# Kernel optimization log

Hardware: AMD Instinct MI355X
Metric: run time of the kernel (lower is better)

Reference implementation:

```python
import jax, jax.numpy as jnp
import numpy as np

IN_C, OUT_C = 128, 256
KH, KW = 3, 3
STRIDE = (1, 1)
PAD = (1, 1)


def setup_inputs() -> dict:
    key = jax.random.key(0)
    kx, kw = jax.random.split(key)
    x = jax.random.normal(kx, (32, IN_C, 56, 56), dtype=jnp.float32)
    k = 1.0 / (IN_C * KH * KW)
    weight = (2.0 * jax.random.uniform(kw, (OUT_C, IN_C, KH, KW), dtype=jnp.float32) - 1.0) * (k ** 0.5)
    return {"x": x, "weight": weight}


def reference(x, weight):
    # Equivalent to the as_strided broadcast-multiply-sum: a plain 2D cross-correlation
    # (no bias), NCHW input, OIHW weight, stride (1,1), padding (1,1).
    return jax.lax.conv_general_dilated(
        x, weight,
        window_strides=STRIDE,
        padding=[(PAD[0], PAD[0]), (PAD[1], PAD[1])],
        dimension_numbers=("NCHW", "OIHW", "NCHW"),
    )
```

## Files before the change

### kernel.cpp

```cpp
#include <hip/hip_runtime.h>

typedef __attribute__((ext_vector_type(8))) short short8;
typedef __attribute__((ext_vector_type(4))) float floatx4;

#define IN_C 128
#define OUT_C 256
#define NB 32
#define HW 56
#define S_PER_N (HW * HW)
#define M_TOTAL (NB * S_PER_N)
#define PH 58
#define PW 66
#define XN_ELEMS (NB * PH * PW * IN_C)
#define WT_ELEMS (9 * OUT_C * IN_C)
#define XF_BLOCKS (PH * NB)
#define WF_BLOCKS (WT_ELEMS / 256)

__device__ __forceinline__ unsigned short f2bf(float f) {
    unsigned int u = __builtin_bit_cast(unsigned int, f);
    u = (u + 0x7FFFu + ((u >> 16) & 1u)) >> 16;
    return (unsigned short)u;
}

__device__ __forceinline__ void gld_lds16(const unsigned short* g, unsigned short* l) {
    __builtin_amdgcn_global_load_lds(
        (const __attribute__((address_space(1))) unsigned int*)g,
        (__attribute__((address_space(3))) unsigned int*)l, 16, 0, 0);
}

__global__ void xform_all(const float* __restrict__ x, const float* __restrict__ w,
                          unsigned short* __restrict__ xn, unsigned short* __restrict__ wt) {
    const int bid = blockIdx.x;
    const int tid = threadIdx.x;

    if (bid >= XF_BLOCKS) {
        const int idx = (bid - XF_BLOCKS) * 256 + tid;
        const int ic  = idx & 127;
        const int oc  = (idx >> 7) & 255;
        const int khw = idx >> 15;
        wt[idx] = f2bf(w[(oc * IN_C + ic) * 9 + khw]);
        return;
    }

    const int ihp = bid % PH;
    const int n   = bid / PH;
    unsigned int* __restrict__ row32 =
        (unsigned int*)(xn + (size_t)(n * PH + ihp) * PW * IN_C);
    const int WORDS = PW * IN_C / 2;

    if (ihp == 0 || ihp == PH - 1) {
        for (int i = tid; i < WORDS; i += 256) row32[i] = 0u;
        return;
    }
    if (tid < 128) {
        int p = (tid >> 6) * (PW - 1);
        row32[p * 64 + (tid & 63)] = 0u;
    }
    const int ih = ihp - 1;
    const float* __restrict__ xrow = x + (size_t)n * IN_C * S_PER_N + (size_t)ih * HW;
#pragma unroll
    for (int t = 0; t < 4; ++t) {
        const int item = tid + t * 256;
        if (item >= 64 * 14) break;
        const int icw  = item & 63;
        const int pix4 = item >> 6;
        const float4 v0 = *(const float4*)(xrow + (size_t)(2 * icw)     * S_PER_N + pix4 * 4);
        const float4 v1 = *(const float4*)(xrow + (size_t)(2 * icw + 1) * S_PER_N + pix4 * 4);
        unsigned int* o = row32 + (pix4 * 4 + 1) * 64 + icw;
        o[0]   = (unsigned int)f2bf(v0.x) | ((unsigned int)f2bf(v1.x) << 16);
        o[64]  = (unsigned int)f2bf(v0.y) | ((unsigned int)f2bf(v1.y) << 16);
        o[128] = (unsigned int)f2bf(v0.z) | ((unsigned int)f2bf(v1.z) << 16);
        o[192] = (unsigned int)f2bf(v0.w) | ((unsigned int)f2bf(v1.w) << 16);
    }
}

__global__ void __launch_bounds__(256, 4)
conv_mfma(const unsigned short* __restrict__ xn,
          const unsigned short* __restrict__ wt,
          float* __restrict__ out) {
    const int tid  = threadIdx.x;
    const int lane = tid & 63;
    const int wv   = tid >> 6;
    const int l15  = lane & 15;
    const int quad = lane >> 4;
    const int fr7  = l15 & 7;

    const int bx0 = blockIdx.x;
    const int bx  = (bx0 & 7) * 196 + (bx0 >> 3);
    const int tile_oc = bx & 1;
    const int tile_m  = bx >> 1;

    const int s_blk  = tile_m * 128;
    const int oc_blk = tile_oc * 128;

    __shared__ unsigned short A_lds[128 * 64];
    __shared__ unsigned short B_lds[128 * 64];

    const int srow = tid >> 3;
    const int sic  = ((tid & 7) ^ (srow & 7)) * 8;

    unsigned int aoff[4], boff[4];
#pragma unroll
    for (int q = 0; q < 4; ++q) {
        int row = q * 32 + srow;
        aoff[q] = (unsigned int)((oc_blk + row) * IN_C + sic);
        int sg = s_blk + row;
        int n  = sg / S_PER_N;
        int r  = sg % S_PER_N;
        int oh = r / HW, ow = r % HW;
        boff[q] = (unsigned int)(((n * PH + oh) * PW + ow) * IN_C + sic);
    }

    const int slot = (quad ^ fr7) * 8;
    const int aof0 = ((wv >> 1) * 64 + l15) * 64 + slot;
    const int bof0 = ((wv & 1)  * 64 + l15) * 64 + slot;

    floatx4 acc[4][4];
#pragma unroll
    for (int i = 0; i < 4; ++i)
#pragma unroll
        for (int j = 0; j < 4; ++j) acc[i][j] = (floatx4){0.f, 0.f, 0.f, 0.f};

#pragma unroll
    for (int khw = 0; khw < 9; ++khw) {
        const int xo = ((khw / 3) * PW + (khw % 3)) * IN_C;
        const int wo = khw * OUT_C * IN_C;
#pragma unroll
        for (int h = 0; h < 2; ++h) {
            const int ic0 = h * 64;
            __syncthreads();
#pragma unroll
            for (int q = 0; q < 4; ++q) {
                gld_lds16(wt + (aoff[q] + (unsigned)(wo + ic0)), A_lds + q * 2048 + tid * 8);
                gld_lds16(xn + (boff[q] + (unsigned)(xo + ic0)), B_lds + q * 2048 + tid * 8);
            }
            __syncthreads();

#pragma unroll
            for (int kk = 0; kk < 2; ++kk) {
                const int ka = aof0 ^ (kk * 32);
                const int kb = bof0 ^ (kk * 32);
                short8 a[4], b[4];
#pragma unroll
                for (int i = 0; i < 4; ++i) a[i] = *(const short8*)(A_lds + ka + i * 1024);
#pragma unroll
                for (int j = 0; j < 4; ++j) b[j] = *(const short8*)(B_lds + kb + j * 1024);
#pragma unroll
                for (int i = 0; i < 4; ++i)
#pragma unroll
                    for (int j = 0; j < 4; ++j)
                        acc[i][j] = __builtin_amdgcn_mfma_f32_16x16x32_bf16(
                            a[i], b[j], acc[i][j], 0, 0, 0);
            }
        }
    }

    const int s0  = s_blk + (wv & 1) * 64;
    const int oc0 = oc_blk + (wv >> 1) * 64;
#pragma unroll
    for (int j = 0; j < 4; ++j) {
        int s_glob = s0 + j * 16 + l15;
        int n = s_glob / S_PER_N;
        int s = s_glob % S_PER_N;
        unsigned int obase = (unsigned int)(n * OUT_C * S_PER_N + s);
#pragma unroll
        for (int i = 0; i < 4; ++i) {
            unsigned int ooff = obase + (unsigned int)((oc0 + i * 16 + quad * 4) * S_PER_N);
#pragma unroll
            for (int r = 0; r < 4; ++r)
                out[ooff + (unsigned int)(r * S_PER_N)] = acc[i][j][r];
        }
    }
}

extern "C" void kernel_launch(void* const* d_in, const int* in_sizes, int n_in,
                              void* d_out, int out_size, void* d_ws, size_t ws_size,
                              hipStream_t stream) {
    const float* x = (const float*)d_in[0];
    const float* w = (const float*)d_in[1];
    float* out = (float*)d_out;

    unsigned short* xn = (unsigned short*)d_ws;
    unsigned short* wt = xn + XN_ELEMS;

    xform_all<<<XF_BLOCKS + WF_BLOCKS, 256, 0, stream>>>(x, w, xn, wt);
    conv_mfma<<<(M_TOTAL / 128) * 2, 256, 0, stream>>>(xn, wt, out);
}
```

Baseline: 203.3 us.

## Prepack weights in MFMA fragment order and load A directly from global

Result: no change. 205.9 us (+1.2%).

```diff
diff --git a/kernel.cpp b/kernel.cpp
--- a/kernel.cpp
+++ b/kernel.cpp
@@ -34,11 +34,18 @@
     const int tid = threadIdx.x;
 
     if (bid >= XF_BLOCKS) {
-        const int idx = (bid - XF_BLOCKS) * 256 + tid;
-        const int ic  = idx & 127;
-        const int oc  = (idx >> 7) & 255;
-        const int khw = idx >> 15;
-        wt[idx] = f2bf(w[(oc * IN_C + ic) * 9 + khw]);
+        const int u     = (bid - XF_BLOCKS) * 256 + tid;
+        const int patch = u >> 9;
+        const int lane  = (u >> 3) & 63;
+        const int e     = u & 7;
+        const int khw   = patch / 64;
+        const int rem   = patch & 63;
+        const int h     = rem >> 5;
+        const int kk    = (rem >> 4) & 1;
+        const int oc16  = rem & 15;
+        const int oc = oc16 * 16 + (lane & 15);
+        const int ic = h * 64 + kk * 32 + (lane >> 4) * 8 + e;
+        wt[u] = f2bf(w[(oc * IN_C + ic) * 9 + khw]);
         return;
     }
 
@@ -93,27 +100,24 @@
     const int s_blk  = tile_m * 128;
     const int oc_blk = tile_oc * 128;
 
-    __shared__ unsigned short A_lds[128 * 64];
     __shared__ unsigned short B_lds[128 * 64];
 
     const int srow = tid >> 3;
     const int sic  = ((tid & 7) ^ (srow & 7)) * 8;
 
-    unsigned int aoff[4], boff[4];
+    unsigned int boff[4];
 #pragma unroll
     for (int q = 0; q < 4; ++q) {
-        int row = q * 32 + srow;
-        aoff[q] = (unsigned int)((oc_blk + row) * IN_C + sic);
-        int sg = s_blk + row;
+        int sg = s_blk + q * 32 + srow;
         int n  = sg / S_PER_N;
         int r  = sg % S_PER_N;
         int oh = r / HW, ow = r % HW;
         boff[q] = (unsigned int)(((n * PH + oh) * PW + ow) * IN_C + sic);
     }
 
-    const int slot = (quad ^ fr7) * 8;
-    const int aof0 = ((wv >> 1) * 64 + l15) * 64 + slot;
-    const int bof0 = ((wv & 1)  * 64 + l15) * 64 + slot;
+    const int bof0 = ((wv & 1) * 64 + l15) * 64 + (quad ^ fr7) * 8;
+    const int pb_wave  = tile_oc * 8 + (wv >> 1) * 4;
+    const unsigned lv8 = (unsigned)(lane * 8);
 
     floatx4 acc[4][4];
 #pragma unroll
@@ -124,25 +128,23 @@
 #pragma unroll
     for (int khw = 0; khw < 9; ++khw) {
         const int xo = ((khw / 3) * PW + (khw % 3)) * IN_C;
-        const int wo = khw * OUT_C * IN_C;
 #pragma unroll
         for (int h = 0; h < 2; ++h) {
             const int ic0 = h * 64;
             __syncthreads();
 #pragma unroll
-            for (int q = 0; q < 4; ++q) {
-                gld_lds16(wt + (aoff[q] + (unsigned)(wo + ic0)), A_lds + q * 2048 + tid * 8);
+            for (int q = 0; q < 4; ++q)
                 gld_lds16(xn + (boff[q] + (unsigned)(xo + ic0)), B_lds + q * 2048 + tid * 8);
-            }
             __syncthreads();
 
 #pragma unroll
             for (int kk = 0; kk < 2; ++kk) {
-                const int ka = aof0 ^ (kk * 32);
-                const int kb = bof0 ^ (kk * 32);
+                const unsigned pbase =
+                    (unsigned)((khw * 64 + h * 32 + kk * 16 + pb_wave) * 512) + lv8;
                 short8 a[4], b[4];
 #pragma unroll
-                for (int i = 0; i < 4; ++i) a[i] = *(const short8*)(A_lds + ka + i * 1024);
+                for (int i = 0; i < 4; ++i) a[i] = *(const short8*)(wt + pbase + i * 512);
+                const int kb = bof0 ^ (kk * 32);
 #pragma unroll
                 for (int j = 0; j < 4; ++j) b[j] = *(const short8*)(B_lds + kb + j * 1024);
 #pragma unroll
```
